# Kernel tuning notes

Hardware: AMD Instinct MI355X
Metric: run time of the kernel (lower is better)

Reference implementation:

```python
import jax, jax.numpy as jnp
import numpy as np

# Assumed constants from the repo's enums
NUM_SPECIAL = 8      # Special.NUM_SPECIAL
CLS_ID = 0           # Special.CLS
CONTEXT_ID = 1       # Special.CONTEXT
NUM_CONTEXT = 16     # Context.NUM_CONTEXT
NUM_BET_BINS = 20
SPECIAL_OFFSET = 52 + NUM_BET_BINS  # get_special_token_offset(num_bet_bins)
D_MODEL = 256
LN_EPS = 1e-5


def setup_inputs() -> dict:
    key = jax.random.key(0)
    ks = jax.random.split(key, 12)
    B, S = 128, 1024
    token_ids = jax.random.randint(ks[0], (B, S), 0, SPECIAL_OFFSET + NUM_SPECIAL)
    context_features = jax.random.normal(ks[1], (B, S, NUM_CONTEXT), dtype=jnp.float32)
    emb_table = jax.random.normal(ks[2], (NUM_SPECIAL, D_MODEL), dtype=jnp.float32)
    W_cls = jax.random.normal(ks[3], (3, D_MODEL), dtype=jnp.float32) / np.sqrt(3.0)
    b_cls = jnp.zeros((D_MODEL,), jnp.float32)
    g_cls = jnp.ones((D_MODEL,), jnp.float32)
    beta_cls = jnp.zeros((D_MODEL,), jnp.float32)
    W_ctx = jax.random.normal(ks[4], (NUM_CONTEXT, D_MODEL), dtype=jnp.float32) / np.sqrt(float(NUM_CONTEXT))
    b_ctx = jnp.zeros((D_MODEL,), jnp.float32)
    g_ctx = jnp.ones((D_MODEL,), jnp.float32)
    beta_ctx = jnp.zeros((D_MODEL,), jnp.float32)
    return {"token_ids": token_ids, "context_features": context_features,
            "emb_table": emb_table,
            "W_cls": W_cls, "b_cls": b_cls, "g_cls": g_cls, "beta_cls": beta_cls,
            "W_ctx": W_ctx, "b_ctx": b_ctx, "g_ctx": g_ctx, "beta_ctx": beta_ctx}


def _mlp(x, W, b, g, beta):
    # Linear -> LayerNorm -> ReLU  (Dropout is identity in eval mode)
    h = x @ W + b                                   # [..., D]
    mu = jnp.mean(h, axis=-1, keepdims=True)
    var = jnp.var(h, axis=-1, keepdims=True)
    h = (h - mu) * jax.lax.rsqrt(var + LN_EPS) * g + beta
    return jax.nn.relu(h)


def reference(token_ids, context_features, emb_table,
              W_cls, b_cls, g_cls, beta_cls,
              W_ctx, b_ctx, g_ctx, beta_ctx):
    special_ids = token_ids - SPECIAL_OFFSET                      # [B,S]
    special_mask = (token_ids >= SPECIAL_OFFSET) & (token_ids < SPECIAL_OFFSET + NUM_SPECIAL)
    safe_ids = jnp.clip(special_ids, 0, NUM_SPECIAL - 1)
    emb = jnp.where(special_mask[..., None], emb_table[safe_ids], 0.0)  # [B,S,D]

    cls_mask = token_ids == SPECIAL_OFFSET + CLS_ID
    cls_out = _mlp(context_features[..., :3], W_cls, b_cls, g_cls, beta_cls)
    emb = emb + jnp.where(cls_mask[..., None], cls_out, 0.0)

    ctx_mask = token_ids == SPECIAL_OFFSET + CONTEXT_ID
    ctx_out = _mlp(context_features, W_ctx, b_ctx, g_ctx, beta_ctx)
    emb = emb + jnp.where(ctx_mask[..., None], ctx_out, 0.0)
    return emb
```

## Files before the change

### kernel.cpp

```cpp
#include <hip/hip_runtime.h>

#define SPECIAL_OFFSET 72
#define NUM_SPECIAL 8
#define D_MODEL 256
#define NUM_CONTEXT 16
#define LN_EPS 1e-5f

__global__ __launch_bounds__(256, 2) void ContextEmbedding_35012573397647_kernel(
    const int*   __restrict__ token_ids,
    const float* __restrict__ ctx_feat,
    const float* __restrict__ emb_table,
    const float* __restrict__ W_cls,
    const float* __restrict__ b_cls,
    const float* __restrict__ g_cls,
    const float* __restrict__ beta_cls,
    const float* __restrict__ W_ctx,
    const float* __restrict__ b_ctx,
    const float* __restrict__ g_ctx,
    const float* __restrict__ beta_ctx,
    float*       __restrict__ out,
    int n_tok)
{
    const int lane          = threadIdx.x & 63;
    const int wave_in_block = threadIdx.x >> 6;
    const int waves_total   = (gridDim.x * blockDim.x) >> 6;
    const int d0            = lane << 2;

    int tok = blockIdx.x * (blockDim.x >> 6) + wave_in_block;
    for (; tok < n_tok; tok += waves_total) {
        const int tid = token_ids[tok];

        float a0 = 0.f, a1 = 0.f, a2 = 0.f, a3 = 0.f;

        if (tid >= SPECIAL_OFFSET && tid < SPECIAL_OFFSET + NUM_SPECIAL) {
            const float4 e = *reinterpret_cast<const float4*>(
                &emb_table[(tid - SPECIAL_OFFSET) * D_MODEL + d0]);
            a0 = e.x; a1 = e.y; a2 = e.z; a3 = e.w;
        }

        if (tid == SPECIAL_OFFSET + 0) {
            const float x0 = ctx_feat[tok * NUM_CONTEXT + 0];
            const float x1 = ctx_feat[tok * NUM_CONTEXT + 1];
            const float x2 = ctx_feat[tok * NUM_CONTEXT + 2];
            const float4 w0 = *reinterpret_cast<const float4*>(&W_cls[0 * D_MODEL + d0]);
            const float4 w1 = *reinterpret_cast<const float4*>(&W_cls[1 * D_MODEL + d0]);
            const float4 w2 = *reinterpret_cast<const float4*>(&W_cls[2 * D_MODEL + d0]);
            const float4 bb = *reinterpret_cast<const float4*>(&b_cls[d0]);
            float h0 = fmaf(x0, w0.x, fmaf(x1, w1.x, fmaf(x2, w2.x, bb.x)));
            float h1 = fmaf(x0, w0.y, fmaf(x1, w1.y, fmaf(x2, w2.y, bb.y)));
            float h2 = fmaf(x0, w0.z, fmaf(x1, w1.z, fmaf(x2, w2.z, bb.z)));
            float h3 = fmaf(x0, w0.w, fmaf(x1, w1.w, fmaf(x2, w2.w, bb.w)));

            float s  = h0 + h1 + h2 + h3;
            float ss = h0 * h0 + h1 * h1 + h2 * h2 + h3 * h3;
            #pragma unroll
            for (int m = 1; m < 64; m <<= 1) {
                s  += __shfl_xor(s,  m, 64);
                ss += __shfl_xor(ss, m, 64);
            }
            const float mu  = s * (1.f / 256.f);
            const float var = ss * (1.f / 256.f) - mu * mu;
            const float inv = rsqrtf(var + LN_EPS);
            const float4 gg = *reinterpret_cast<const float4*>(&g_cls[d0]);
            const float4 be = *reinterpret_cast<const float4*>(&beta_cls[d0]);
            a0 += fmaxf((h0 - mu) * inv * gg.x + be.x, 0.f);
            a1 += fmaxf((h1 - mu) * inv * gg.y + be.y, 0.f);
            a2 += fmaxf((h2 - mu) * inv * gg.z + be.z, 0.f);
            a3 += fmaxf((h3 - mu) * inv * gg.w + be.w, 0.f);
        }

        if (tid == SPECIAL_OFFSET + 1) {
            const float4 bb = *reinterpret_cast<const float4*>(&b_ctx[d0]);
            float h0 = bb.x, h1 = bb.y, h2 = bb.z, h3 = bb.w;
            #pragma unroll
            for (int k = 0; k < NUM_CONTEXT; ++k) {
                const float xk = ctx_feat[tok * NUM_CONTEXT + k];
                const float4 w = *reinterpret_cast<const float4*>(&W_ctx[k * D_MODEL + d0]);
                h0 = fmaf(xk, w.x, h0);
                h1 = fmaf(xk, w.y, h1);
                h2 = fmaf(xk, w.z, h2);
                h3 = fmaf(xk, w.w, h3);
            }
            float s  = h0 + h1 + h2 + h3;
            float ss = h0 * h0 + h1 * h1 + h2 * h2 + h3 * h3;
            #pragma unroll
            for (int m = 1; m < 64; m <<= 1) {
                s  += __shfl_xor(s,  m, 64);
                ss += __shfl_xor(ss, m, 64);
            }
            const float mu  = s * (1.f / 256.f);
            const float var = ss * (1.f / 256.f) - mu * mu;
            const float inv = rsqrtf(var + LN_EPS);
            const float4 gg = *reinterpret_cast<const float4*>(&g_ctx[d0]);
            const float4 be = *reinterpret_cast<const float4*>(&beta_ctx[d0]);
            a0 += fmaxf((h0 - mu) * inv * gg.x + be.x, 0.f);
            a1 += fmaxf((h1 - mu) * inv * gg.y + be.y, 0.f);
            a2 += fmaxf((h2 - mu) * inv * gg.z + be.z, 0.f);
            a3 += fmaxf((h3 - mu) * inv * gg.w + be.w, 0.f);
        }

        float4 o; o.x = a0; o.y = a1; o.z = a2; o.w = a3;
        *reinterpret_cast<float4*>(&out[tok * D_MODEL + d0]) = o;
    }
}

extern "C" void kernel_launch(void* const* d_in, const int* in_sizes, int n_in,
                              void* d_out, int out_size, void* d_ws, size_t ws_size,
                              hipStream_t stream) {
    const int*   token_ids = (const int*)  d_in[0];
    const float* ctx_feat  = (const float*)d_in[1];
    const float* emb_table = (const float*)d_in[2];
    const float* W_cls     = (const float*)d_in[3];
    const float* b_cls     = (const float*)d_in[4];
    const float* g_cls     = (const float*)d_in[5];
    const float* beta_cls  = (const float*)d_in[6];
    const float* W_ctx     = (const float*)d_in[7];
    const float* b_ctx     = (const float*)d_in[8];
    const float* g_ctx     = (const float*)d_in[9];
    const float* beta_ctx  = (const float*)d_in[10];
    float* out = (float*)d_out;

    const int n_tok = in_sizes[0];
    const int block = 256;
    const int waves_needed = n_tok;
    int grid = (waves_needed + 3) / 4;
    if (grid > 2048) grid = 2048;

    ContextEmbedding_35012573397647_kernel<<<grid, block, 0, stream>>>(
        token_ids, ctx_feat, emb_table,
        W_cls, b_cls, g_cls, beta_cls,
        W_ctx, b_ctx, g_ctx, beta_ctx,
        out, n_tok);
}
```

Baseline: 27.88 us.

## Batch 16 tokens per wave with shuffled ids, outlined MLP paths, nontemporal stores

```diff
diff --git a/kernel.cpp b/kernel.cpp
--- a/kernel.cpp
+++ b/kernel.cpp
@@ -5,102 +5,133 @@
 #define D_MODEL 256
 #define NUM_CONTEXT 16
 #define LN_EPS 1e-5f
+#define TOK_PER_WAVE 16
 
-__global__ __launch_bounds__(256, 2) void ContextEmbedding_35012573397647_kernel(
+typedef float vfloat4 __attribute__((ext_vector_type(4)));
+
+
+__device__ __noinline__ float4 mlp_cls_path(const float* __restrict__ xf,
+                                            const float* __restrict__ W,
+                                            const float* __restrict__ b,
+                                            const float* __restrict__ g,
+                                            const float* __restrict__ be,
+                                            int d0)
+{
+    const float x0 = xf[0], x1 = xf[1], x2 = xf[2];
+    const float4 w0 = *reinterpret_cast<const float4*>(&W[0 * D_MODEL + d0]);
+    const float4 w1 = *reinterpret_cast<const float4*>(&W[1 * D_MODEL + d0]);
+    const float4 w2 = *reinterpret_cast<const float4*>(&W[2 * D_MODEL + d0]);
+    const float4 bb = *reinterpret_cast<const float4*>(&b[d0]);
+    float h0 = fmaf(x0, w0.x, fmaf(x1, w1.x, fmaf(x2, w2.x, bb.x)));
+    float h1 = fmaf(x0, w0.y, fmaf(x1, w1.y, fmaf(x2, w2.y, bb.y)));
+    float h2 = fmaf(x0, w0.z, fmaf(x1, w1.z, fmaf(x2, w2.z, bb.z)));
+    float h3 = fmaf(x0, w0.w, fmaf(x1, w1.w, fmaf(x2, w2.w, bb.w)));
+
+    float s  = h0 + h1 + h2 + h3;
+    float ss = h0 * h0 + h1 * h1 + h2 * h2 + h3 * h3;
+    #pragma unroll
+    for (int m = 1; m < 64; m <<= 1) {
+        s  += __shfl_xor(s,  m, 64);
+        ss += __shfl_xor(ss, m, 64);
+    }
+    const float mu  = s * (1.f / 256.f);
+    const float var = ss * (1.f / 256.f) - mu * mu;
+    const float inv = rsqrtf(var + LN_EPS);
+    const float4 gg = *reinterpret_cast<const float4*>(&g[d0]);
+    const float4 bt = *reinterpret_cast<const float4*>(&be[d0]);
+    float4 r;
+    r.x = fmaxf((h0 - mu) * inv * gg.x + bt.x, 0.f);
+    r.y = fmaxf((h1 - mu) * inv * gg.y + bt.y, 0.f);
+    r.z = fmaxf((h2 - mu) * inv * gg.z + bt.z, 0.f);
+    r.w = fmaxf((h3 - mu) * inv * gg.w + bt.w, 0.f);
+    return r;
+}
+
+__device__ __noinline__ float4 mlp_ctx_path(const float* __restrict__ xf,
+                                            const float* __restrict__ W,
+                                            const float* __restrict__ b,
+                                            const float* __restrict__ g,
+                                            const float* __restrict__ be,
+                                            int d0)
+{
+    const float4 bb = *reinterpret_cast<const float4*>(&b[d0]);
+    float h0 = bb.x, h1 = bb.y, h2 = bb.z, h3 = bb.w;
+    #pragma unroll
+    for (int k = 0; k < NUM_CONTEXT; ++k) {
+        const float xk = xf[k];
+        const float4 w = *reinterpret_cast<const float4*>(&W[k * D_MODEL + d0]);
+        h0 = fmaf(xk, w.x, h0);
+        h1 = fmaf(xk, w.y, h1);
+        h2 = fmaf(xk, w.z, h2);
+        h3 = fmaf(xk, w.w, h3);
+    }
+    float s  = h0 + h1 + h2 + h3;
+    float ss = h0 * h0 + h1 * h1 + h2 * h2 + h3 * h3;
+    #pragma unroll
+    for (int m = 1; m < 64; m <<= 1) {
+        s  += __shfl_xor(s,  m, 64);
+        ss += __shfl_xor(ss, m, 64);
+    }
+    const float mu  = s * (1.f / 256.f);
+    const float var = ss * (1.f / 256.f) - mu * mu;
+    const float inv = rsqrtf(var + LN_EPS);
+    const float4 gg = *reinterpret_cast<const float4*>(&g[d0]);
+    const float4 bt = *reinterpret_cast<const float4*>(&be[d0]);
+    float4 r;
+    r.x = fmaxf((h0 - mu) * inv * gg.x + bt.x, 0.f);
+    r.y = fmaxf((h1 - mu) * inv * gg.y + bt.y, 0.f);
+    r.z = fmaxf((h2 - mu) * inv * gg.z + bt.z, 0.f);
+    r.w = fmaxf((h3 - mu) * inv * gg.w + bt.w, 0.f);
+    return r;
+}
+
+__global__ __launch_bounds__(256, 8) void ContextEmbedding_35012573397647_kernel(
     const int*   __restrict__ token_ids,
     const float* __restrict__ ctx_feat,
     const float* __restrict__ emb_table,
-    const float* __restrict__ W_cls,
-    const float* __restrict__ b_cls,
-    const float* __restrict__ g_cls,
-    const float* __restrict__ beta_cls,
-    const float* __restrict__ W_ctx,
-    const float* __restrict__ b_ctx,
-    const float* __restrict__ g_ctx,
-    const float* __restrict__ beta_ctx,
+    const float* __restrict__ W_cls, const float* __restrict__ b_cls,
+    const float* __restrict__ g_cls, const float* __restrict__ beta_cls,
+    const float* __restrict__ W_ctx, const float* __restrict__ b_ctx,
+    const float* __restrict__ g_ctx, const float* __restrict__ beta_ctx,
     float*       __restrict__ out,
     int n_tok)
 {
-    const int lane          = threadIdx.x & 63;
-    const int wave_in_block = threadIdx.x >> 6;
-    const int waves_total   = (gridDim.x * blockDim.x) >> 6;
-    const int d0            = lane << 2;
+    const int lane        = threadIdx.x & 63;
+    const int wave_in_blk = threadIdx.x >> 6;
+    const int waves_total = (gridDim.x * blockDim.x) >> 6;
+    const int d0          = lane << 2;
+    const int n_batch     = (n_tok + TOK_PER_WAVE - 1) / TOK_PER_WAVE;
 
-    int tok = blockIdx.x * (blockDim.x >> 6) + wave_in_block;
-    for (; tok < n_tok; tok += waves_total) {
-        const int tid = token_ids[tok];
+    for (int batch = blockIdx.x * 4 + wave_in_blk; batch < n_batch; batch += waves_total) {
+        const int tok_base = batch * TOK_PER_WAVE;
 
-        float a0 = 0.f, a1 = 0.f, a2 = 0.f, a3 = 0.f;
+        const int idx = tok_base + (lane & 15);
+        const int myid = (idx < n_tok) ? token_ids[idx] : -1;
 
-        if (tid >= SPECIAL_OFFSET && tid < SPECIAL_OFFSET + NUM_SPECIAL) {
-            const float4 e = *reinterpret_cast<const float4*>(
-                &emb_table[(tid - SPECIAL_OFFSET) * D_MODEL + d0]);
-            a0 = e.x; a1 = e.y; a2 = e.z; a3 = e.w;
+        #pragma unroll
+        for (int i = 0; i < TOK_PER_WAVE; ++i) {
+            const int tok = tok_base + i;
+            if (tok >= n_tok) break;
+            const int tid = __shfl(myid, i, 16);
+
+            float4 o; o.x = 0.f; o.y = 0.f; o.z = 0.f; o.w = 0.f;
+            if (tid >= SPECIAL_OFFSET && tid < SPECIAL_OFFSET + NUM_SPECIAL) {
+                o = *reinterpret_cast<const float4*>(
+                    &emb_table[(tid - SPECIAL_OFFSET) * D_MODEL + d0]);
+                if (tid == SPECIAL_OFFSET + 0) {
+                    const float4 m = mlp_cls_path(&ctx_feat[(size_t)tok * NUM_CONTEXT],
+                                                  W_cls, b_cls, g_cls, beta_cls, d0);
+                    o.x += m.x; o.y += m.y; o.z += m.z; o.w += m.w;
+                } else if (tid == SPECIAL_OFFSET + 1) {
+                    const float4 m = mlp_ctx_path(&ctx_feat[(size_t)tok * NUM_CONTEXT],
+                                                  W_ctx, b_ctx, g_ctx, beta_ctx, d0);
+                    o.x += m.x; o.y += m.y; o.z += m.z; o.w += m.w;
+                }
+            }
+            vfloat4 ov; ov.x = o.x; ov.y = o.y; ov.z = o.z; ov.w = o.w;
+            __builtin_nontemporal_store(ov, reinterpret_cast<vfloat4*>(
+                &out[(size_t)tok * D_MODEL + d0]));
         }
-
-        if (tid == SPECIAL_OFFSET + 0) {
-            const float x0 = ctx_feat[tok * NUM_CONTEXT + 0];
-            const float x1 = ctx_feat[tok * NUM_CONTEXT + 1];
-            const float x2 = ctx_feat[tok * NUM_CONTEXT + 2];
-            const float4 w0 = *reinterpret_cast<const float4*>(&W_cls[0 * D_MODEL + d0]);
-            const float4 w1 = *reinterpret_cast<const float4*>(&W_cls[1 * D_MODEL + d0]);
-            const float4 w2 = *reinterpret_cast<const float4*>(&W_cls[2 * D_MODEL + d0]);
-            const float4 bb = *reinterpret_cast<const float4*>(&b_cls[d0]);
-            float h0 = fmaf(x0, w0.x, fmaf(x1, w1.x, fmaf(x2, w2.x, bb.x)));
-            float h1 = fmaf(x0, w0.y, fmaf(x1, w1.y, fmaf(x2, w2.y, bb.y)));
-            float h2 = fmaf(x0, w0.z, fmaf(x1, w1.z, fmaf(x2, w2.z, bb.z)));
-            float h3 = fmaf(x0, w0.w, fmaf(x1, w1.w, fmaf(x2, w2.w, bb.w)));
-
-            float s  = h0 + h1 + h2 + h3;
-            float ss = h0 * h0 + h1 * h1 + h2 * h2 + h3 * h3;
-            #pragma unroll
-            for (int m = 1; m < 64; m <<= 1) {
-                s  += __shfl_xor(s,  m, 64);
-                ss += __shfl_xor(ss, m, 64);
-            }
-            const float mu  = s * (1.f / 256.f);
-            const float var = ss * (1.f / 256.f) - mu * mu;
-            const float inv = rsqrtf(var + LN_EPS);
-            const float4 gg = *reinterpret_cast<const float4*>(&g_cls[d0]);
-            const float4 be = *reinterpret_cast<const float4*>(&beta_cls[d0]);
-            a0 += fmaxf((h0 - mu) * inv * gg.x + be.x, 0.f);
-            a1 += fmaxf((h1 - mu) * inv * gg.y + be.y, 0.f);
-            a2 += fmaxf((h2 - mu) * inv * gg.z + be.z, 0.f);
-            a3 += fmaxf((h3 - mu) * inv * gg.w + be.w, 0.f);
-        }
-
-        if (tid == SPECIAL_OFFSET + 1) {
-            const float4 bb = *reinterpret_cast<const float4*>(&b_ctx[d0]);
-            float h0 = bb.x, h1 = bb.y, h2 = bb.z, h3 = bb.w;
-            #pragma unroll
-            for (int k = 0; k < NUM_CONTEXT; ++k) {
-                const float xk = ctx_feat[tok * NUM_CONTEXT + k];
-                const float4 w = *reinterpret_cast<const float4*>(&W_ctx[k * D_MODEL + d0]);
-                h0 = fmaf(xk, w.x, h0);
-                h1 = fmaf(xk, w.y, h1);
-                h2 = fmaf(xk, w.z, h2);
-                h3 = fmaf(xk, w.w, h3);
-            }
-            float s  = h0 + h1 + h2 + h3;
-            float ss = h0 * h0 + h1 * h1 + h2 * h2 + h3 * h3;
-            #pragma unroll
-            for (int m = 1; m < 64; m <<= 1) {
-                s  += __shfl_xor(s,  m, 64);
-                ss += __shfl_xor(ss, m, 64);
-            }
-            const float mu  = s * (1.f / 256.f);
-            const float var = ss * (1.f / 256.f) - mu * mu;
-            const float inv = rsqrtf(var + LN_EPS);
-            const float4 gg = *reinterpret_cast<const float4*>(&g_ctx[d0]);
-            const float4 be = *reinterpret_cast<const float4*>(&beta_ctx[d0]);
-            a0 += fmaxf((h0 - mu) * inv * gg.x + be.x, 0.f);
-            a1 += fmaxf((h1 - mu) * inv * gg.y + be.y, 0.f);
-            a2 += fmaxf((h2 - mu) * inv * gg.z + be.z, 0.f);
-            a3 += fmaxf((h3 - mu) * inv * gg.w + be.w, 0.f);
-        }
-
-        float4 o; o.x = a0; o.y = a1; o.z = a2; o.w = a3;
-        *reinterpret_cast<float4*>(&out[tok * D_MODEL + d0]) = o;
     }
 }
 
@@ -120,13 +151,12 @@
     const float* beta_ctx  = (const float*)d_in[10];
     float* out = (float*)d_out;
 
-    const int n_tok = in_sizes[0];
-    const int block = 256;
-    const int waves_needed = n_tok;
-    int grid = (waves_needed + 3) / 4;
+    const int n_tok   = in_sizes[0];
+    const int n_batch = (n_tok + TOK_PER_WAVE - 1) / TOK_PER_WAVE;
+    int grid = (n_batch + 3) / 4;
     if (grid > 2048) grid = 2048;
 
-    ContextEmbedding_35012573397647_kernel<<<grid, block, 0, stream>>>(
+    ContextEmbedding_35012573397647_kernel<<<grid, 256, 0, stream>>>(
         token_ids, ctx_feat, emb_table,
         W_cls, b_cls, g_cls, beta_cls,
         W_ctx, b_ctx, g_ctx, beta_ctx,
```

Measured after the change: 35.59 us. 1.28x slower.
